# Kernel optimization log

Measured on AMD Instinct MI355X. Metric: run time of the kernel, lower is better.

The kernel has to match this reference:

```python
import jax, jax.numpy as jnp
import numpy as np

H = 1024      # hidden_dim
NH = 16       # num_heads
HD = H // NH  # head_dim
FFN = 4096
EPS = 1e-5


def setup_inputs() -> dict:
    key = jax.random.key(0)
    ks = jax.random.split(key, 12)
    s = 0.02
    return {
        "x": jax.random.normal(ks[0], (2, 2048, H), dtype=jnp.float32),
        "w_qkv": jax.random.normal(ks[1], (H, 3 * H), dtype=jnp.float32) * s,
        "b_qkv": jnp.zeros((3 * H,), dtype=jnp.float32),
        "w_out": jax.random.normal(ks[2], (H, H), dtype=jnp.float32) * s,
        "b_out": jnp.zeros((H,), dtype=jnp.float32),
        "ln1_g": jnp.ones((H,), dtype=jnp.float32),
        "ln1_b": jnp.zeros((H,), dtype=jnp.float32),
        "ln2_g": jnp.ones((H,), dtype=jnp.float32),
        "ln2_b": jnp.zeros((H,), dtype=jnp.float32),
        "w1": jax.random.normal(ks[3], (H, FFN), dtype=jnp.float32) * s,
        "b1": jnp.zeros((FFN,), dtype=jnp.float32),
        "w2": jax.random.normal(ks[4], (FFN, H), dtype=jnp.float32) * s,
        "b2": jnp.zeros((H,), dtype=jnp.float32),
    }


def _layernorm(x, g, b):
    mu = jnp.mean(x, axis=-1, keepdims=True)
    var = jnp.mean(jnp.square(x - mu), axis=-1, keepdims=True)
    return (x - mu) * jax.lax.rsqrt(var + EPS) * g + b


def reference(x, w_qkv, b_qkv, w_out, b_out, ln1_g, ln1_b, ln2_g, ln2_b, w1, b1, w2, b2):
    B, S, _ = x.shape
    # pre-LN attention branch
    h = _layernorm(x, ln1_g, ln1_b)
    qkv = h @ w_qkv + b_qkv                       # (B,S,3H)
    qkv = qkv.reshape(B, S, 3, NH, HD).transpose(2, 0, 3, 1, 4)
    q, k, v = qkv[0], qkv[1], qkv[2]              # (B,NH,S,HD)
    scores = jnp.einsum("bhqd,bhkd->bhqk", q, k) / jnp.sqrt(jnp.float32(HD))
    causal = jnp.triu(jnp.ones((S, S), dtype=bool), k=1)
    scores = jnp.where(causal, -jnp.inf, scores)
    attn = jax.nn.softmax(scores, axis=-1)
    out = jnp.einsum("bhqk,bhkd->bhqd", attn, v)  # (B,NH,S,HD)
    out = out.transpose(0, 2, 1, 3).reshape(B, S, H)
    attn_out = out @ w_out + b_out
    x = x + attn_out
    # FFN branch
    h2 = _layernorm(x, ln2_g, ln2_b)
    ffn = jax.nn.gelu(h2 @ w1 + b1, approximate=False) @ w2 + b2
    return x + ffn
```

## Files before the change

### kernel.cpp

```cpp
#include <hip/hip_runtime.h>
#include <hip/hip_bf16.h>

typedef __bf16 bf16_t;
typedef __bf16 bf16x8 __attribute__((ext_vector_type(8)));
typedef __bf16 bf16x4 __attribute__((ext_vector_type(4)));
typedef __bf16 bf16x2 __attribute__((ext_vector_type(2)));
typedef float  f32x4  __attribute__((ext_vector_type(4)));

#define HDIM 1024
#define SEQ  2048
#define NHEAD 16
#define HEADD 64

__device__ __forceinline__ void gld_lds16(const void* g, void* l) {
  __builtin_amdgcn_global_load_lds(
      (const __attribute__((address_space(1))) unsigned int*)g,
      (__attribute__((address_space(3))) unsigned int*)l, 16, 0, 0);
}

__global__ __launch_bounds__(256) void ln_kernel(const float* __restrict__ x,
                                                 const float* __restrict__ gam,
                                                 const float* __restrict__ bet,
                                                 bf16_t* __restrict__ out) {
  int row = blockIdx.x;
  int t = threadIdx.x;
  const float4* xr = (const float4*)(x + (size_t)row * HDIM);
  float4 v = xr[t];
  float s = v.x + v.y + v.z + v.w;
  float ss = v.x*v.x + v.y*v.y + v.z*v.z + v.w*v.w;
  #pragma unroll
  for (int o = 32; o > 0; o >>= 1) {
    s  += __shfl_xor(s, o);
    ss += __shfl_xor(ss, o);
  }
  __shared__ float red[8];
  int w = t >> 6;
  if ((t & 63) == 0) { red[w*2] = s; red[w*2+1] = ss; }
  __syncthreads();
  s  = red[0] + red[2] + red[4] + red[6];
  ss = red[1] + red[3] + red[5] + red[7];
  float mu  = s * (1.0f / HDIM);
  float var = ss * (1.0f / HDIM) - mu * mu;
  float rstd = rsqrtf(var + 1e-5f);
  float4 g4 = ((const float4*)gam)[t];
  float4 b4 = ((const float4*)bet)[t];
  bf16x4 o4;
  o4[0] = (bf16_t)((v.x - mu) * rstd * g4.x + b4.x);
  o4[1] = (bf16_t)((v.y - mu) * rstd * g4.y + b4.y);
  o4[2] = (bf16_t)((v.z - mu) * rstd * g4.z + b4.z);
  o4[3] = (bf16_t)((v.w - mu) * rstd * g4.w + b4.w);
  *(bf16x4*)(out + (size_t)row * HDIM + t * 4) = o4;
}

__global__ __launch_bounds__(256) void transpose_cast(const float* __restrict__ W,
                                                      bf16_t* __restrict__ Wt,
                                                      int Kd, int Nd) {
  __shared__ float tile[32][33];
  int n0 = blockIdx.x * 32, k0 = blockIdx.y * 32;
  int tx = threadIdx.x & 31, ty = threadIdx.x >> 5;
  #pragma unroll
  for (int i = 0; i < 4; i++)
    tile[ty + i*8][tx] = W[(size_t)(k0 + ty + i*8) * Nd + n0 + tx];
  __syncthreads();
  #pragma unroll
  for (int i = 0; i < 4; i++)
    Wt[(size_t)(n0 + ty + i*8) * Kd + k0 + tx] = (bf16_t)tile[tx][ty + i*8];
}

__device__ __forceinline__ float gelu_fast(float x) {
  float y = 0.7978845608f * (x + 0.044715f * x * x * x);
  float u = exp2f(y * 2.885390082f);
  float th = 1.0f - 2.0f * __builtin_amdgcn_rcpf(u + 1.0f);
  return 0.5f * x * (1.0f + th);
}

__global__ __launch_bounds__(256)
void reduce2_kernel(const bf16_t* __restrict__ p0, const bf16_t* __restrict__ p1,
                    const float* __restrict__ bias, const float* __restrict__ resid,
                    float* __restrict__ out) {
  size_t base = ((size_t)blockIdx.x * 256 + threadIdx.x) * 8;
  bf16x8 a = *(const bf16x8*)(p0 + base);
  bf16x8 b = *(const bf16x8*)(p1 + base);
  int col = (int)(base & (HDIM - 1));
  float4 bi0 = *(const float4*)(bias + col);
  float4 bi1 = *(const float4*)(bias + col + 4);
  float4 r0 = *(const float4*)(resid + base);
  float4 r1 = *(const float4*)(resid + base + 4);
  float4 o0, o1;
  o0.x = (float)a[0] + (float)b[0] + bi0.x + r0.x;
  o0.y = (float)a[1] + (float)b[1] + bi0.y + r0.y;
  o0.z = (float)a[2] + (float)b[2] + bi0.z + r0.z;
  o0.w = (float)a[3] + (float)b[3] + bi0.w + r0.w;
  o1.x = (float)a[4] + (float)b[4] + bi1.x + r1.x;
  o1.y = (float)a[5] + (float)b[5] + bi1.y + r1.y;
  o1.z = (float)a[6] + (float)b[6] + bi1.z + r1.z;
  o1.w = (float)a[7] + (float)b[7] + bi1.w + r1.w;
  *(float4*)(out + base)     = o0;
  *(float4*)(out + base + 4) = o1;
}

template<int EPI, int BN, int SPLITK>
__global__ __launch_bounds__(256, 2)
void gemm_bt(const bf16_t* __restrict__ A, const bf16_t* __restrict__ Bt,
             const float* __restrict__ bias, const float* __restrict__ resid,
             void* __restrict__ outp, int M, int N, int K) {
  constexpr int NFRAG = BN / 32;
  __shared__ bf16_t As[2][128*64];
  __shared__ bf16_t Bs[2][BN*64];
  int t = threadIdx.x;
  int w = t >> 6, l = t & 63;
  int wr = w >> 1, wc = w & 1;

  int nbx = gridDim.x;
  int bid = blockIdx.y * nbx + blockIdx.x;
  int chunkx = (nbx * gridDim.y) >> 3;
  int nb = (bid & 7) * chunkx + (bid >> 3);
  int bm = nb / nbx, bn = nb % nbx;
  size_t m0 = (size_t)bm * 128, n0 = (size_t)bn * BN;

  const int KK = (SPLITK > 1) ? K / SPLITK : K;
  const size_t koff = (SPLITK > 1) ? (size_t)blockIdx.z * KK : 0;

  f32x4 acc[4][NFRAG];
  #pragma unroll
  for (int m = 0; m < 4; m++)
    #pragma unroll
    for (int n = 0; n < NFRAG; n++) acc[m][n] = (f32x4)(0.0f);

  int srow = t >> 3;
  int scol = ((t & 7) ^ (srow & 7)) * 8;
  int dsto = t * 8;
  const bf16_t* ag = A  + (m0 + srow) * K + koff + scol;
  const bf16_t* bg = Bt + (n0 + srow) * K + koff + scol;

  int lr = l & 15, lg = l >> 4;

  auto stage = [&](int buf, int k0) {
    #pragma unroll
    for (int p = 0; p < 4; p++)
      gld_lds16(ag + k0 + (size_t)(p*32)*K, &As[buf][dsto + p*32*64]);
    #pragma unroll
    for (int p = 0; p < BN/32; p++)
      gld_lds16(bg + k0 + (size_t)(p*32)*K, &Bs[buf][dsto + p*32*64]);
  };

  stage(0, 0);
  __syncthreads();
  int cur = 0;
  const int NK = KK / 64;
  for (int k = 0; k < NK; k++) {
    if (k + 1 < NK) stage(cur ^ 1, (k + 1) * 64);
    #pragma unroll
    for (int kk = 0; kk < 2; kk++) {
      bf16x8 af[4], bfr[NFRAG];
      #pragma unroll
      for (int m = 0; m < 4; m++) {
        int row = wr*64 + m*16 + lr;
        int off = row*128 + (((kk*4 + lg) ^ (row & 7)) << 4);
        af[m] = *(const bf16x8*)((const char*)&As[cur][0] + off);
      }
      #pragma unroll
      for (int n = 0; n < NFRAG; n++) {
        int row = wc*(BN/2) + n*16 + lr;
        int off = row*128 + (((kk*4 + lg) ^ (row & 7)) << 4);
        bfr[n] = *(const bf16x8*)((const char*)&Bs[cur][0] + off);
      }
      #pragma unroll
      for (int m = 0; m < 4; m++)
        #pragma unroll
        for (int n = 0; n < NFRAG; n++)
          acc[m][n] = __builtin_amdgcn_mfma_f32_16x16x32_bf16(af[m], bfr[n], acc[m][n], 0, 0, 0);
    }
    __syncthreads();
    cur ^= 1;
  }

  int r0 = (l >> 4) * 4, c0 = l & 15;
  bf16_t* pd = nullptr;
  if (EPI == 3)
    pd = (bf16_t*)(blockIdx.z == 0 ? outp : (void*)resid);
  #pragma unroll
  for (int m = 0; m < 4; m++) {
    #pragma unroll
    for (int n = 0; n < NFRAG; n++) {
      size_t row = m0 + wr*64 + m*16 + r0;
      size_t col = n0 + wc*(BN/2) + n*16 + c0;
      float bv = (EPI == 3) ? 0.0f : bias[col];
      #pragma unroll
      for (int r = 0; r < 4; r++) {
        float vv = acc[m][n][r] + bv;
        size_t idx = (row + r) * (size_t)N + col;
        if (EPI == 0) {
          ((bf16_t*)outp)[idx] = (bf16_t)vv;
        } else if (EPI == 1) {
          ((float*)outp)[idx] = vv + resid[idx];
        } else if (EPI == 2) {
          ((bf16_t*)outp)[idx] = (bf16_t)gelu_fast(vv);
        } else {
          pd[idx] = (bf16_t)vv;
        }
      }
    }
  }
}

__global__ __launch_bounds__(512, 4)
void attn_kernel(const bf16_t* __restrict__ qkv, bf16_t* __restrict__ out) {
  int idx = blockIdx.x;
  int half = idx >> 8;
  int sub = idx & 255;
  int qth = sub >> 5;
  int qt = half ? qth : (15 - qth);
  int bh = sub & 31;
  int b = bh >> 4, h = bh & 15;
  int t = threadIdx.x, w = t >> 6, l = t & 63;

  __shared__ bf16_t Ks[2][64*64];
  __shared__ bf16_t Vt[2][64*72];
  __shared__ bf16_t Ps[8][16*64];

  const size_t RS = 3 * HDIM;
  const bf16_t* qb = qkv + (size_t)b * SEQ * RS + h * HEADD;
  const bf16_t* kb = qb + HDIM;
  const bf16_t* vb = qb + 2 * HDIM;

  int lr = l & 15, lg = l >> 4;
  const float SCALE = 0.125f * 1.44269504f;

  bf16x8 qf[2];
  {
    size_t qrow = (size_t)qt * 128 + w * 16 + lr;
    qf[0] = *(const bf16x8*)(qb + qrow * RS + lg * 8);
    qf[1] = *(const bf16x8*)(qb + qrow * RS + 32 + lg * 8);
    #pragma unroll
    for (int i = 0; i < 8; i++) {
      qf[0][i] = (bf16_t)((float)qf[0][i] * SCALE);
      qf[1][i] = (bf16_t)((float)qf[1][i] * SCALE);
    }
  }

  f32x4 o[4];
  #pragma unroll
  for (int d = 0; d < 4; d++) o[d] = (f32x4)(0.0f);
  float m = -1e30f, lsum = 0.0f;

  int srow = t >> 3, scol = (t & 7) * 8;
  int Fv = ((scol >> 3) & 7) << 3;
  int nkt = 2 * qt + 2;

  const bf16_t* kg0 = kb + (size_t)srow * RS + scol;
  const bf16_t* vg0 = vb + (size_t)srow * RS + scol;

  bf16x8 kr = *(const bf16x8*)kg0;
  bf16x8 vr = *(const bf16x8*)vg0;

  int wrow0 = qt * 128 + w * 16;
  int qg = wrow0 + lr;
  bf16_t* pw = Ps[w];
  int psw = (lr & 7) << 4;
  int cur = 0;

  for (int kt = 0; kt < nkt; kt++) {
    {
      int ba = srow * 128 + scol * 2;
      int sw = (srow & 7) << 4;
      *(bf16x8*)((char*)Ks[cur] + (ba ^ sw)) = kr;
      int ksw = srow ^ Fv;
      bf16_t* vt = Vt[cur];
      #pragma unroll
      for (int i = 0; i < 8; i++)
        vt[(scol + i) * 72 + ksw] = vr[i];
    }
    if (kt + 1 < nkt) {
      kr = *(const bf16x8*)(kg0 + (size_t)(kt + 1) * 64 * RS);
      vr = *(const bf16x8*)(vg0 + (size_t)(kt + 1) * 64 * RS);
    }
    asm volatile("s_waitcnt lgkmcnt(0)" ::: "memory");
    __builtin_amdgcn_s_barrier();
    __builtin_amdgcn_sched_barrier(0);

    bool skipw = (kt * 64) > (wrow0 + 15);
    if (!skipw) {
      f32x4 sc[4];
      __builtin_amdgcn_s_setprio(1);
      #pragma unroll
      for (int kt2 = 0; kt2 < 4; kt2++) {
        sc[kt2] = (f32x4)(0.0f);
        #pragma unroll
        for (int kk = 0; kk < 2; kk++) {
          int row = kt2 * 16 + lr;
          int off = (row * 128 + kk * 64 + lg * 16) ^ ((row & 7) << 4);
          bf16x8 kf = *(const bf16x8*)((char*)Ks[cur] + off);
          sc[kt2] = __builtin_amdgcn_mfma_f32_16x16x32_bf16(kf, qf[kk], sc[kt2], 0, 0, 0);
        }
      }
      __builtin_amdgcn_s_setprio(0);
      if (kt * 64 + 63 > wrow0) {
        #pragma unroll
        for (int kt2 = 0; kt2 < 4; kt2++) {
          #pragma unroll
          for (int r = 0; r < 4; r++) {
            int kcol = kt*64 + kt2*16 + lg*4 + r;
            if (kcol > qg) sc[kt2][r] = -1e30f;
          }
        }
      }
      float tm0 = fmaxf(fmaxf(sc[0][0], sc[0][1]), fmaxf(sc[0][2], sc[0][3]));
      float tm1 = fmaxf(fmaxf(sc[1][0], sc[1][1]), fmaxf(sc[1][2], sc[1][3]));
      float tm2 = fmaxf(fmaxf(sc[2][0], sc[2][1]), fmaxf(sc[2][2], sc[2][3]));
      float tm3 = fmaxf(fmaxf(sc[3][0], sc[3][1]), fmaxf(sc[3][2], sc[3][3]));
      float tm = fmaxf(fmaxf(tm0, tm1), fmaxf(tm2, tm3));
      tm = fmaxf(tm, __shfl_xor(tm, 16));
      tm = fmaxf(tm, __shfl_xor(tm, 32));
      if (!__all(tm <= m + 8.0f)) {
        float nm = fmaxf(m, tm);
        float alpha = exp2f(m - nm);
        m = nm;
        lsum *= alpha;
        #pragma unroll
        for (int d = 0; d < 4; d++)
          #pragma unroll
          for (int r = 0; r < 4; r++) o[d][r] *= alpha;
      }
      #pragma unroll
      for (int kt2 = 0; kt2 < 4; kt2++) {
        float p0 = exp2f(sc[kt2][0] - m);
        float p1 = exp2f(sc[kt2][1] - m);
        float p2 = exp2f(sc[kt2][2] - m);
        float p3 = exp2f(sc[kt2][3] - m);
        lsum += (p0 + p1) + (p2 + p3);
        bf16x2 pa; pa[0] = (bf16_t)p0; pa[1] = (bf16_t)p1;
        bf16x2 pb; pb[0] = (bf16_t)p2; pb[1] = (bf16_t)p3;
        int base = lr * 128 + kt2 * 32 + lg * 8;
        *(bf16x2*)((char*)pw + ((base)     ^ psw)) = pa;
        *(bf16x2*)((char*)pw + ((base + 4) ^ psw)) = pb;
      }
      asm volatile("s_waitcnt lgkmcnt(0)" ::: "memory");
      __builtin_amdgcn_s_setprio(1);
      #pragma unroll
      for (int kk = 0; kk < 2; kk++) {
        int poff = (lr * 128 + kk * 64 + lg * 16) ^ psw;
        bf16x8 pf = *(const bf16x8*)((char*)pw + poff);
        #pragma unroll
        for (int dblk = 0; dblk < 4; dblk++) {
          int vrow = dblk * 16 + lr;
          int Fd = ((vrow >> 3) & 7) << 3;
          bf16x8 vf = *(const bf16x8*)(Vt[cur] + vrow * 72 + ((kk * 32 + lg * 8) ^ Fd));
          o[dblk] = __builtin_amdgcn_mfma_f32_16x16x32_bf16(vf, pf, o[dblk], 0, 0, 0);
        }
      }
      __builtin_amdgcn_s_setprio(0);
    }
    cur ^= 1;
  }

  lsum += __shfl_xor(lsum, 16);
  lsum += __shfl_xor(lsum, 32);
  float inv = 1.0f / lsum;

  bf16_t* ob = out + ((size_t)b * SEQ + qg) * HDIM + h * HEADD;
  #pragma unroll
  for (int dblk = 0; dblk < 4; dblk++) {
    bf16x4 q4;
    #pragma unroll
    for (int r = 0; r < 4; r++) q4[r] = (bf16_t)(o[dblk][r] * inv);
    *(bf16x4*)(ob + dblk * 16 + lg * 4) = q4;
  }
}

extern "C" void kernel_launch(void* const* d_in, const int* in_sizes, int n_in,
                              void* d_out, int out_size, void* d_ws, size_t ws_size,
                              hipStream_t stream) {
  (void)in_sizes; (void)n_in; (void)out_size; (void)ws_size;
  const float* x     = (const float*)d_in[0];
  const float* w_qkv = (const float*)d_in[1];
  const float* b_qkv = (const float*)d_in[2];
  const float* w_out = (const float*)d_in[3];
  const float* b_out = (const float*)d_in[4];
  const float* ln1_g = (const float*)d_in[5];
  const float* ln1_b = (const float*)d_in[6];
  const float* ln2_g = (const float*)d_in[7];
  const float* ln2_b = (const float*)d_in[8];
  const float* w1    = (const float*)d_in[9];
  const float* b1    = (const float*)d_in[10];
  const float* w2    = (const float*)d_in[11];
  const float* b2    = (const float*)d_in[12];
  float* out = (float*)d_out;

  char* ws = (char*)d_ws;
  size_t off = 0;
  auto alloc = [&](size_t bytes) -> void* {
    void* p = ws + off;
    off += (bytes + 255) & ~(size_t)255;
    return p;
  };
  bf16_t* wqkvT = (bf16_t*)alloc((size_t)3072*1024*2);
  bf16_t* woutT = (bf16_t*)alloc((size_t)1024*1024*2);
  bf16_t* w1T   = (bf16_t*)alloc((size_t)4096*1024*2);
  bf16_t* w2T   = (bf16_t*)alloc((size_t)1024*4096*2);
  bf16_t* ln1o  = (bf16_t*)alloc((size_t)4096*1024*2);
  bf16_t* qkvb  = (bf16_t*)alloc((size_t)4096*4096*2);
  bf16_t* attno = (bf16_t*)alloc((size_t)4096*1024*2);
  float*  x2    = (float*) alloc((size_t)4096*1024*4);
  bf16_t* h2 = ln1o;
  bf16_t* g  = qkvb;
  bf16_t* part0 = ln1o;
  bf16_t* part1 = attno;

  dim3 blk(256);
  transpose_cast<<<dim3(3072/32, 1024/32), blk, 0, stream>>>(w_qkv, wqkvT, 1024, 3072);
  transpose_cast<<<dim3(1024/32, 1024/32), blk, 0, stream>>>(w_out, woutT, 1024, 1024);
  transpose_cast<<<dim3(4096/32, 1024/32), blk, 0, stream>>>(w1,    w1T,   1024, 4096);
  transpose_cast<<<dim3(1024/32, 4096/32), blk, 0, stream>>>(w2,    w2T,   4096, 1024);

  ln_kernel<<<4096, blk, 0, stream>>>(x, ln1_g, ln1_b, ln1o);
  gemm_bt<0,128,1><<<dim3(24, 32), blk, 0, stream>>>(ln1o, wqkvT, b_qkv, nullptr, qkvb, 4096, 3072, 1024);
  attn_kernel<<<512, dim3(512), 0, stream>>>(qkvb, attno);
  gemm_bt<1,64,1><<<dim3(16, 32), blk, 0, stream>>>(attno, woutT, b_out, x, x2, 4096, 1024, 1024);
  ln_kernel<<<4096, blk, 0, stream>>>(x2, ln2_g, ln2_b, h2);
  gemm_bt<2,128,1><<<dim3(32, 32), blk, 0, stream>>>(h2, w1T, b1, nullptr, g, 4096, 4096, 1024);
  gemm_bt<3,128,2><<<dim3(8, 32, 2), blk, 0, stream>>>(g, w2T, b2, (const float*)part1, part0, 4096, 1024, 4096);
  reduce2_kernel<<<2048, blk, 0, stream>>>(part0, part1, b2, x2, out);
}
```

Before: 230.6 us.

## Parametrize GEMM K-tile and occupancy; use raw exp2 intrinsic in attention and GELU

The GEMM template now takes the K-tile depth and waves-per-EU as parameters. The LDS swizzle and staging pattern are generalized so BK=32 works. The QKV and FFN1 GEMMs use BK=32 with a launch bound of 4 to halve shared memory and raise occupancy, at the cost of more barriers per K step and possibly register spills. Separately, exp2f calls in softmax and GELU are replaced with the hardware exp2 builtin to skip the library's range handling.

```diff
diff --git a/kernel.cpp b/kernel.cpp
--- a/kernel.cpp
+++ b/kernel.cpp
@@ -16,6 +16,14 @@
   __builtin_amdgcn_global_load_lds(
       (const __attribute__((address_space(1))) unsigned int*)g,
       (__attribute__((address_space(3))) unsigned int*)l, 16, 0, 0);
+}
+
+__device__ __forceinline__ float fexp2(float x) {
+#if __has_builtin(__builtin_amdgcn_exp2f)
+  return __builtin_amdgcn_exp2f(x);
+#else
+  return exp2f(x);
+#endif
 }
 
 __global__ __launch_bounds__(256) void ln_kernel(const float* __restrict__ x,
@@ -69,7 +77,7 @@
 
 __device__ __forceinline__ float gelu_fast(float x) {
   float y = 0.7978845608f * (x + 0.044715f * x * x * x);
-  float u = exp2f(y * 2.885390082f);
+  float u = fexp2(y * 2.885390082f);
   float th = 1.0f - 2.0f * __builtin_amdgcn_rcpf(u + 1.0f);
   return 0.5f * x * (1.0f + th);
 }
@@ -99,14 +107,18 @@
   *(float4*)(out + base + 4) = o1;
 }
 
-template<int EPI, int BN, int SPLITK>
-__global__ __launch_bounds__(256, 2)
+template<int EPI, int BN, int BK, int WPEU, int SPLITK>
+__global__ __launch_bounds__(256, WPEU)
 void gemm_bt(const bf16_t* __restrict__ A, const bf16_t* __restrict__ Bt,
              const float* __restrict__ bias, const float* __restrict__ resid,
              void* __restrict__ outp, int M, int N, int K) {
   constexpr int NFRAG = BN / 32;
-  __shared__ bf16_t As[2][128*64];
-  __shared__ bf16_t Bs[2][BN*64];
+  constexpr int CH  = BK / 8;
+  constexpr int SWZ = CH - 1;
+  constexpr int RSH = (BK == 32) ? 1 : 0;
+  constexpr int RPP = 256 / CH;
+  __shared__ bf16_t As[2][128*BK];
+  __shared__ bf16_t Bs[2][BN*BK];
   int t = threadIdx.x;
   int w = t >> 6, l = t & 63;
   int wr = w >> 1, wc = w & 1;
@@ -127,8 +139,8 @@
     #pragma unroll
     for (int n = 0; n < NFRAG; n++) acc[m][n] = (f32x4)(0.0f);
 
-  int srow = t >> 3;
-  int scol = ((t & 7) ^ (srow & 7)) * 8;
+  int srow = t / CH;
+  int scol = ((t & SWZ) ^ ((srow >> RSH) & SWZ)) * 8;
   int dsto = t * 8;
   const bf16_t* ag = A  + (m0 + srow) * K + koff + scol;
   const bf16_t* bg = Bt + (n0 + srow) * K + koff + scol;
@@ -137,32 +149,32 @@
 
   auto stage = [&](int buf, int k0) {
     #pragma unroll
-    for (int p = 0; p < 4; p++)
-      gld_lds16(ag + k0 + (size_t)(p*32)*K, &As[buf][dsto + p*32*64]);
-    #pragma unroll
-    for (int p = 0; p < BN/32; p++)
-      gld_lds16(bg + k0 + (size_t)(p*32)*K, &Bs[buf][dsto + p*32*64]);
+    for (int p = 0; p < 128/RPP; p++)
+      gld_lds16(ag + k0 + (size_t)(p*RPP)*K, &As[buf][dsto + p*RPP*BK]);
+    #pragma unroll
+    for (int p = 0; p < BN/RPP; p++)
+      gld_lds16(bg + k0 + (size_t)(p*RPP)*K, &Bs[buf][dsto + p*RPP*BK]);
   };
 
   stage(0, 0);
   __syncthreads();
   int cur = 0;
-  const int NK = KK / 64;
+  const int NK = KK / BK;
   for (int k = 0; k < NK; k++) {
-    if (k + 1 < NK) stage(cur ^ 1, (k + 1) * 64);
-    #pragma unroll
-    for (int kk = 0; kk < 2; kk++) {
+    if (k + 1 < NK) stage(cur ^ 1, (k + 1) * BK);
+    #pragma unroll
+    for (int kk = 0; kk < BK/32; kk++) {
       bf16x8 af[4], bfr[NFRAG];
       #pragma unroll
       for (int m = 0; m < 4; m++) {
         int row = wr*64 + m*16 + lr;
-        int off = row*128 + (((kk*4 + lg) ^ (row & 7)) << 4);
+        int off = row*BK*2 + (((kk*4 + lg) ^ ((row >> RSH) & SWZ)) << 4);
         af[m] = *(const bf16x8*)((const char*)&As[cur][0] + off);
       }
       #pragma unroll
       for (int n = 0; n < NFRAG; n++) {
         int row = wc*(BN/2) + n*16 + lr;
-        int off = row*128 + (((kk*4 + lg) ^ (row & 7)) << 4);
+        int off = row*BK*2 + (((kk*4 + lg) ^ ((row >> RSH) & SWZ)) << 4);
         bfr[n] = *(const bf16x8*)((const char*)&Bs[cur][0] + off);
       }
       #pragma unroll
@@ -314,7 +326,7 @@
       tm = fmaxf(tm, __shfl_xor(tm, 32));
       if (!__all(tm <= m + 8.0f)) {
         float nm = fmaxf(m, tm);
-        float alpha = exp2f(m - nm);
+        float alpha = fexp2(m - nm);
         m = nm;
         lsum *= alpha;
         #pragma unroll
@@ -324,10 +336,10 @@
       }
       #pragma unroll
       for (int kt2 = 0; kt2 < 4; kt2++) {
-        float p0 = exp2f(sc[kt2][0] - m);
-        float p1 = exp2f(sc[kt2][1] - m);
-        float p2 = exp2f(sc[kt2][2] - m);
-        float p3 = exp2f(sc[kt2][3] - m);
+        float p0 = fexp2(sc[kt2][0] - m);
+        float p1 = fexp2(sc[kt2][1] - m);
+        float p2 = fexp2(sc[kt2][2] - m);
+        float p3 = fexp2(sc[kt2][3] - m);
         lsum += (p0 + p1) + (p2 + p3);
         bf16x2 pa; pa[0] = (bf16_t)p0; pa[1] = (bf16_t)p1;
         bf16x2 pb; pb[0] = (bf16_t)p2; pb[1] = (bf16_t)p3;
@@ -414,11 +426,11 @@
   transpose_cast<<<dim3(1024/32, 4096/32), blk, 0, stream>>>(w2,    w2T,   4096, 1024);
 
   ln_kernel<<<4096, blk, 0, stream>>>(x, ln1_g, ln1_b, ln1o);
-  gemm_bt<0,128,1><<<dim3(24, 32), blk, 0, stream>>>(ln1o, wqkvT, b_qkv, nullptr, qkvb, 4096, 3072, 1024);
+  gemm_bt<0,128,32,4,1><<<dim3(24, 32), blk, 0, stream>>>(ln1o, wqkvT, b_qkv, nullptr, qkvb, 4096, 3072, 1024);
   attn_kernel<<<512, dim3(512), 0, stream>>>(qkvb, attno);
-  gemm_bt<1,64,1><<<dim3(16, 32), blk, 0, stream>>>(attno, woutT, b_out, x, x2, 4096, 1024, 1024);
+  gemm_bt<1,64,64,2,1><<<dim3(16, 32), blk, 0, stream>>>(attno, woutT, b_out, x, x2, 4096, 1024, 1024);
   ln_kernel<<<4096, blk, 0, stream>>>(x2, ln2_g, ln2_b, h2);
-  gemm_bt<2,128,1><<<dim3(32, 32), blk, 0, stream>>>(h2, w1T, b1, nullptr, g, 4096, 4096, 1024);
-  gemm_bt<3,128,2><<<dim3(8, 32, 2), blk, 0, stream>>>(g, w2T, b2, (const float*)part1, part0, 4096, 1024, 4096);
+  gemm_bt<2,128,32,4,1><<<dim3(32, 32), blk, 0, stream>>>(h2, w1T, b1, nullptr, g, 4096, 4096, 1024);
+  gemm_bt<3,128,64,2,2><<<dim3(8, 32, 2), blk, 0, stream>>>(g, w2T, b2, (const float*)part1, part0, 4096, 1024, 4096);
   reduce2_kernel<<<2048, blk, 0, stream>>>(part0, part1, b2, x2, out);
 }
```

Result: faster. 217.5 us (-5.7%).
